# Kernel tuning notes

Measured on AMD Instinct MI355X. Metric: run time of the kernel, lower is better.

The kernel has to match this reference:

```python
import jax, jax.numpy as jnp
import numpy as np

GROUPS = 8
N_HEADS = 8
EPS = 1e-5


def setup_inputs() -> dict:
    key = jax.random.key(0)
    ks = jax.random.split(key, 3)
    B, C, H, W = 8, 512, 32, 32
    x = jax.random.normal(ks[0], (B, C, H, W), dtype=jnp.float32)
    # Conv2d(C, 3C, 1) weight squeezed to [3C, C]; kaiming-ish scale
    qkv_w = jax.random.normal(ks[1], (3 * C, C), dtype=jnp.float32) * (1.0 / np.sqrt(C))
    proj_w = jax.random.normal(ks[2], (C, C), dtype=jnp.float32) * (1.0 / np.sqrt(C))
    return {
        "x": x,
        "norm_gamma": jnp.ones((C,), jnp.float32),
        "norm_beta": jnp.zeros((C,), jnp.float32),
        "qkv_w": qkv_w,
        "qkv_b": jnp.zeros((3 * C,), jnp.float32),
        "proj_w": proj_w,
        "proj_b": jnp.zeros((C,), jnp.float32),
    }


def reference(x, norm_gamma, norm_beta, qkv_w, qkv_b, proj_w, proj_b):
    B, C, H, W = x.shape
    nh = N_HEADS
    hd = C // nh
    scale = hd ** (-0.5)
    S = H * W

    # GroupNorm(8, C): normalize over (C/G, H, W) within each group
    xg = x.reshape(B, GROUPS, -1)
    mean = xg.mean(axis=-1, keepdims=True)
    var = xg.var(axis=-1, keepdims=True)
    xn = ((xg - mean) * jax.lax.rsqrt(var + EPS)).reshape(B, C, H, W)
    xn = xn * norm_gamma[None, :, None, None] + norm_beta[None, :, None, None]

    # 1x1 conv QKV == per-pixel matmul
    qkv = jnp.einsum('oc,bchw->bohw', qkv_w, xn) + qkv_b[None, :, None, None]
    qkv = qkv.reshape(B, 3, nh, hd, S)
    q, k, v = qkv[:, 0], qkv[:, 1], qkv[:, 2]  # each (B, nh, hd, S)

    # attn[b,h,s,t] = sum_d q[b,h,d,s] k[b,h,d,t] * scale
    attn = jax.nn.softmax(jnp.einsum('bhds,bhdt->bhst', q, k) * scale, axis=-1)
    out = jnp.einsum('bhst,bhdt->bhds', attn, v).reshape(B, C, H, W)

    # 1x1 conv projection + residual
    return x + jnp.einsum('oc,bchw->bohw', proj_w, out) + proj_b[None, :, None, None]
```

## Files before the change

kernel.cpp:

```cpp
#include <hip/hip_runtime.h>
#include <hip/hip_bf16.h>

typedef __attribute__((ext_vector_type(4))) float  f32x4;
typedef __attribute__((ext_vector_type(8))) _Float16 f16x8;
typedef __attribute__((ext_vector_type(4))) _Float16 f16x4;
typedef __attribute__((ext_vector_type(2))) __fp16 fp16x2;
typedef __attribute__((ext_vector_type(4))) float  float4v;
typedef __attribute__((ext_vector_type(4))) unsigned int uint4v;

#define BATCH   8
#define CDIM    512
#define SLEN    1024
#define NHEADS  8
#define HDIM    64
#define QSCALE  0.1803368801111f
#define FIXED_M 8.0f


__device__ __forceinline__ float fast_exp2(float x){
    float r;
    asm("v_exp_f32 %0, %1" : "=v"(r) : "v"(x));
    return r;
}

__device__ __forceinline__ void stage16(const void* g, void* l, int lane){
#if __has_builtin(__builtin_amdgcn_global_load_lds)
    __builtin_amdgcn_global_load_lds((const __attribute__((address_space(1))) void*)g,
                                     (__attribute__((address_space(3))) void*)l, 16, 0, 0);
#else
    *(f16x8*)((char*)l + lane * 16) = *(const f16x8*)g;
#endif
}

__device__ __forceinline__ int sigma32(int p){
    return 8 * ((p >> 2) & 3) + 4 * ((p >> 4) & 1) + (p & 3);
}

union PB8 { fp16x2 q[4]; f16x8 v; };


__global__ __launch_bounds__(256) void prep(
    const float4v* __restrict__ qkvw, f16x4* __restrict__ wq,
    const float4v* __restrict__ projw, f16x4* __restrict__ pw,
    const float* __restrict__ x, float* __restrict__ part)
{
    __shared__ float s1[256], s2[256];
    if (blockIdx.x < 1024){
        int i = blockIdx.x * 256 + threadIdx.x;
        if (i < 196608){
            float4v v = qkvw[i];
            wq[i] = (f16x4){ (_Float16)v[0], (_Float16)v[1], (_Float16)v[2], (_Float16)v[3] };
        } else {
            int j = i - 196608;
            float4v v = projw[j];
            pw[j] = (f16x4){ (_Float16)v[0], (_Float16)v[1], (_Float16)v[2], (_Float16)v[3] };
        }
        return;
    }
    int bid = blockIdx.x - 1024;
    int bg = bid >> 3, pc = bid & 7;
    const float4v* xp = (const float4v*)(x + (size_t)bg * 65536 + (size_t)pc * 8192);
    float sum = 0.f, sq = 0.f;
    for (int i = threadIdx.x; i < 2048; i += 256){
        float4v v = xp[i];
        sum += (v[0] + v[1]) + (v[2] + v[3]);
        sq  += (v[0]*v[0] + v[1]*v[1]) + (v[2]*v[2] + v[3]*v[3]);
    }
    s1[threadIdx.x] = sum; s2[threadIdx.x] = sq;
    __syncthreads();
    for (int o = 128; o > 0; o >>= 1){
        if (threadIdx.x < o){ s1[threadIdx.x] += s1[threadIdx.x + o];
                              s2[threadIdx.x] += s2[threadIdx.x + o]; }
        __syncthreads();
    }
    if (threadIdx.x == 0){
        part[bid * 2 + 0] = s1[0];
        part[bid * 2 + 1] = s2[0];
    }
}


__global__ __launch_bounds__(256) void gn_apply(
    const float* __restrict__ x, const float* __restrict__ part,
    const float* __restrict__ gamma, const float* __restrict__ beta,
    _Float16* __restrict__ xnT)
{
    int b = blockIdx.z, g = blockIdx.y, s0 = blockIdx.x * 64;
    int bg = b * 8 + g, c0 = g * 64;

    float sum = 0.f, sq = 0.f;
#pragma unroll
    for (int p = 0; p < 8; p++){
        sum += part[bg * 16 + p * 2 + 0];
        sq  += part[bg * 16 + p * 2 + 1];
    }
    float mean = sum * (1.f / 65536.f);
    float var  = sq  * (1.f / 65536.f) - mean * mean;
    float inv  = rsqrtf(var + 1e-5f);

    __shared__ _Float16 tile[64 * 66];

    int tx = threadIdx.x & 15, ty = threadIdx.x >> 4;
#pragma unroll
    for (int j = 0; j < 4; j++){
        int c = ty + 16 * j;
        float ga = gamma[c0 + c] * inv;
        float be = beta[c0 + c] - mean * ga;
        float4v v = *(const float4v*)(x + ((size_t)(b * CDIM + c0 + c)) * SLEN + s0 + tx * 4);
#pragma unroll
        for (int i = 0; i < 4; i++)
            tile[(tx * 4 + i) * 66 + c] = (_Float16)(v[i] * ga + be);
    }
    __syncthreads();

    int s = threadIdx.x >> 2, cq = (threadIdx.x & 3) * 16;
    const unsigned int* lsrc = (const unsigned int*)((const unsigned short*)tile + s * 66 + cq);
    uint4v lo = { lsrc[0], lsrc[1], lsrc[2], lsrc[3] };
    uint4v hi = { lsrc[4], lsrc[5], lsrc[6], lsrc[7] };
    unsigned int* dst = (unsigned int*)(xnT + ((size_t)b * SLEN + s0 + s) * CDIM + c0 + cq);
    *(uint4v*)dst       = lo;
    *(uint4v*)(dst + 4) = hi;
}


#define GEMM_CORE(APTR, BPTR)                                                   \
    __shared__ __align__(16) char smem[34816];                                  \
    int tid = threadIdx.x;                                                      \
    int wid = tid >> 6, lane = tid & 63;                                        \
    int w0 = wid >> 1, w1 = wid & 1;                                            \
    int lr = lane & 15, lg = lane >> 4;                                         \
    int slotg = ((lane & 3) ^ ((lane >> 3) & 3)) * 16;                          \
    int srow = lane >> 2;                                                       \
    const char* agp = (const char*)(APTR) +                                     \
        ((size_t)(bo + wid * 32 + srow) * CDIM) * 2 + slotg;                    \
    const char* bgp = (const char*)(BPTR) +                                     \
        ((size_t)(sgbase + wid * 32 + srow) * CDIM) * 2 + slotg;                \
    char* lA = smem + wid * 2048;                                               \
    char* lB = smem + 8192 + wid * 2048;                                        \
    f32x4 acc[4][4];                                                            \
    _Pragma("unroll") for (int i = 0; i < 4; i++)                               \
    _Pragma("unroll") for (int j = 0; j < 4; j++)                               \
        acc[i][j] = (f32x4){0.f, 0.f, 0.f, 0.f};                                \
    _Pragma("unroll") for (int j = 0; j < 2; j++){                              \
        stage16(agp + j * 16384, lA + j * 1024, lane);                          \
        stage16(bgp + j * 16384, lB + j * 1024, lane);                          \
    }                                                                           \
    __syncthreads();                                                            \
    int xt = ((lr >> 1) & 3) << 4;                                              \
    for (int it = 0; it < 16; ++it){                                            \
        int cur = (it & 1) * 16384;                                             \
        if (it + 1 < 16){                                                       \
            int nxt = 16384 - cur, ko = (it + 1) * 64;                          \
            _Pragma("unroll") for (int j = 0; j < 2; j++){                      \
                stage16(agp + j * 16384 + ko, lA + nxt + j * 1024, lane);       \
                stage16(bgp + j * 16384 + ko, lB + nxt + j * 1024, lane);       \
            }                                                                   \
        }                                                                       \
        const char* Ac = smem + cur + (w0 * 64 + lr) * 64;                      \
        const char* Bc = smem + cur + 8192 + (w1 * 64 + lr) * 64;               \
        f16x8 af[4], bfr[4];                                                    \
        _Pragma("unroll") for (int t = 0; t < 4; t++){                          \
            af[t]  = *(const f16x8*)(Ac + t * 1024 + ((lg * 16) ^ xt));         \
            bfr[t] = *(const f16x8*)(Bc + t * 1024 + ((lg * 16) ^ xt));         \
        }                                                                       \
        _Pragma("unroll") for (int i = 0; i < 4; i++)                           \
        _Pragma("unroll") for (int j = 0; j < 4; j++)                           \
            acc[i][j] = __builtin_amdgcn_mfma_f32_16x16x32_f16(af[i], bfr[j],   \
                                                               acc[i][j], 0, 0, 0); \
        __syncthreads();                                                        \
    }


__global__ __launch_bounds__(256) void qkv_gemm(
    const _Float16* __restrict__ wq, const _Float16* __restrict__ xnT,
    const float* __restrict__ qkvb,
    _Float16* __restrict__ qT, _Float16* __restrict__ kT, _Float16* __restrict__ vv)
{
    int b  = blockIdx.z;
    int bo = blockIdx.y * 128;
    size_t sgbase = (size_t)b * SLEN + blockIdx.x * 128;

    GEMM_CORE(wq, xnT)

    int obase = bo + w0 * 64, sbase = blockIdx.x * 128 + w1 * 64;
    int p = obase >> 9;
    int h = (obase >> 6) & 7;
    size_t bh = (size_t)b * NHEADS + h;

    if (p == 2){
        _Float16* vt = (_Float16*)(smem + wid * 8704);
#pragma unroll
        for (int i = 0; i < 4; i++){
            int d0 = i * 16 + lg * 4;
            float4v bias = *(const float4v*)(qkvb + obase + d0);
#pragma unroll
            for (int j = 0; j < 4; j++){
                int s_loc = j * 16 + lr;
#pragma unroll
                for (int r = 0; r < 4; r++)
                    vt[(d0 + r) * 68 + s_loc] = (_Float16)(acc[i][j][r] + bias[r]);
            }
        }
        asm volatile("" ::: "memory");
        _Float16* dstv = vv + (bh * HDIM) * SLEN + sbase;
        int dl = lane >> 3, sc8 = (lane & 7) * 8;
#pragma unroll
        for (int m = 0; m < 8; m++){
            int d = m * 8 + dl;
            f16x8 row = *(const f16x8*)(vt + d * 68 + sc8);
            *(f16x8*)(dstv + (size_t)d * SLEN + sc8) = row;
        }
    } else {
        float sc = (p == 0) ? QSCALE : 1.f;
        char* wreg = smem + wid * 8192;
#pragma unroll
        for (int i = 0; i < 4; i++){
            int d0 = i * 16 + lg * 4;
            float4v bias = *(const float4v*)(qkvb + obase + d0);
            int slotbase = (2 * i + (lg >> 1)) * 16;
            int inoff = (lg & 1) * 8;
#pragma unroll
            for (int j = 0; j < 4; j++){
                int s_loc = j * 16 + lr;
                f16x4 pk = { (_Float16)((acc[i][j][0] + bias[0]) * sc),
                             (_Float16)((acc[i][j][1] + bias[1]) * sc),
                             (_Float16)((acc[i][j][2] + bias[2]) * sc),
                             (_Float16)((acc[i][j][3] + bias[3]) * sc) };
                *(f16x4*)(wreg + s_loc * 128 + (slotbase ^ ((s_loc & 7) << 4)) + inoff) = pk;
            }
        }
        asm volatile("" ::: "memory");
        _Float16* dst = (p == 0 ? qT : kT) + (bh * SLEN + sbase) * HDIM;
#pragma unroll
        for (int m = 0; m < 8; m++){
            int s_loc = m * 8 + (lane >> 3);
            f16x8 row = *(const f16x8*)(wreg + s_loc * 128 + (((lane & 7) ^ (s_loc & 7)) << 4));
            *(f16x8*)(dst + (size_t)s_loc * HDIM + (lane & 7) * 8) = row;
        }
    }
}


__global__ __launch_bounds__(256) void proj_gemm(
    const _Float16* __restrict__ pw, const _Float16* __restrict__ outT,
    const float* __restrict__ pb, const float* __restrict__ x,
    float* __restrict__ y)
{
    int b  = blockIdx.z;
    int bo = blockIdx.y * 128;
    size_t sgbase = (size_t)b * SLEN + blockIdx.x * 128;

    GEMM_CORE(pw, outT)

    int obase = bo + w0 * 64, sbase = blockIdx.x * 128 + w1 * 64;
    float* wreg = (float*)(smem + wid * 8704);

#pragma unroll
    for (int half = 0; half < 2; half++){
        asm volatile("" ::: "memory");
#pragma unroll
        for (int jj = 0; jj < 2; jj++){
            int j = half * 2 + jj;
            int srow2 = jj * 16 + lr;
#pragma unroll
            for (int i = 0; i < 4; i++){
                int c0 = i * 16 + lg * 4;
                float4v bias = *(const float4v*)(pb + obase + c0);
                float4v v = { acc[i][j][0] + bias[0], acc[i][j][1] + bias[1],
                              acc[i][j][2] + bias[2], acc[i][j][3] + bias[3] };
                *(float4v*)(wreg + srow2 * 68 + c0) = v;
            }
        }
        asm volatile("" ::: "memory");
        int cl = lane >> 3, sq = (lane & 7) * 4;
#pragma unroll
        for (int g = 0; g < 8; g++){
            int c = cl + 8 * g;
            float r0 = wreg[(sq + 0) * 68 + c];
            float r1 = wreg[(sq + 1) * 68 + c];
            float r2 = wreg[(sq + 2) * 68 + c];
            float r3 = wreg[(sq + 3) * 68 + c];
            size_t idx = ((size_t)b * CDIM + obase + c) * SLEN + sbase + half * 32 + sq;
            float4v xr = *(const float4v*)(x + idx);
            float4v o = { r0 + xr[0], r1 + xr[1], r2 + xr[2], r3 + xr[3] };
            *(float4v*)(y + idx) = o;
        }
    }
}


#define ATTN_CHUNK(c)                                                           \
    {                                                                           \
        const char* kbuf = smem + ((c) & 3) * 16384;                            \
        const char* vbuf = kbuf + 8192;                                         \
        f16x8 kf[4][2];                                                         \
        _Pragma("unroll") for (int i = 0; i < 4; i++){                          \
            const char* kr = kbuf + (16 * i + lr) * 128;                        \
            kf[i][0] = *(const f16x8*)(kr + ((lg * 16) ^ r7));                  \
            kf[i][1] = *(const f16x8*)(kr + ((64 + lg * 16) ^ r7));             \
        }                                                                       \
        f16x8 vf8[2][4];                                                        \
        _Pragma("unroll") for (int ip = 0; ip < 2; ip++)                        \
        _Pragma("unroll") for (int dt = 0; dt < 4; dt++)                        \
            vf8[ip][dt] = *(const f16x8*)(vbuf + (dt * 16 + lr) * 128           \
                                          + ((ip * 64 + lg * 16) ^ r7));        \
        _Pragma("unroll") for (int sj = 0; sj < 2; sj++){                       \
            f32x4 st[4];                                                        \
            _Pragma("unroll") for (int i = 0; i < 4; i++){                      \
                f32x4 z = (f32x4){-FIXED_M, -FIXED_M, -FIXED_M, -FIXED_M};      \
                z = __builtin_amdgcn_mfma_f32_16x16x32_f16(kf[i][0], qf[sj][0], z, 0, 0, 0); \
                z = __builtin_amdgcn_mfma_f32_16x16x32_f16(kf[i][1], qf[sj][1], z, 0, 0, 0); \
                st[i] = z;                                                      \
            }                                                                   \
            PB8 ua, ub;                                                         \
            ua.q[0] = __builtin_amdgcn_cvt_pkrtz(fast_exp2(st[0][0]), fast_exp2(st[0][1])); \
            ua.q[1] = __builtin_amdgcn_cvt_pkrtz(fast_exp2(st[0][2]), fast_exp2(st[0][3])); \
            ua.q[2] = __builtin_amdgcn_cvt_pkrtz(fast_exp2(st[1][0]), fast_exp2(st[1][1])); \
            ua.q[3] = __builtin_amdgcn_cvt_pkrtz(fast_exp2(st[1][2]), fast_exp2(st[1][3])); \
            ub.q[0] = __builtin_amdgcn_cvt_pkrtz(fast_exp2(st[2][0]), fast_exp2(st[2][1])); \
            ub.q[1] = __builtin_amdgcn_cvt_pkrtz(fast_exp2(st[2][2]), fast_exp2(st[2][3])); \
            ub.q[2] = __builtin_amdgcn_cvt_pkrtz(fast_exp2(st[3][0]), fast_exp2(st[3][1])); \
            ub.q[3] = __builtin_amdgcn_cvt_pkrtz(fast_exp2(st[3][2]), fast_exp2(st[3][3])); \
            f16x8 pb8_0 = ua.v, pb8_1 = ub.v;                                   \
            osum[sj] = __builtin_amdgcn_mfma_f32_16x16x32_f16(ones8, pb8_0, osum[sj], 0, 0, 0); \
            osum[sj] = __builtin_amdgcn_mfma_f32_16x16x32_f16(ones8, pb8_1, osum[sj], 0, 0, 0); \
            _Pragma("unroll") for (int dt = 0; dt < 4; dt++){                   \
                f32x4 o = oac[dt][sj];                                          \
                o = __builtin_amdgcn_mfma_f32_16x16x32_f16(vf8[0][dt], pb8_0, o, 0, 0, 0); \
                o = __builtin_amdgcn_mfma_f32_16x16x32_f16(vf8[1][dt], pb8_1, o, 0, 0, 0); \
                oac[dt][sj] = o;                                                \
            }                                                                   \
        }                                                                       \
    }

__global__ __launch_bounds__(256) void attn_kernel(
    const _Float16* __restrict__ qT, const _Float16* __restrict__ kT,
    const _Float16* __restrict__ vv, _Float16* __restrict__ outT)
{
    __shared__ __align__(16) char smem[65536];

    int id = blockIdx.x;
    int h = id & 7, rr = id >> 3;
    int sx = rr & 7, b = rr >> 3;
    size_t bh = (size_t)b * NHEADS + h;
    int tid = threadIdx.x;
    int wid = tid >> 6, lane = tid & 63;
    int lr = lane & 15, lg = lane >> 4;
    int sbase = sx * 128 + wid * 32;
    int phase = sx << 1;

    const _Float16* qp = qT + bh * SLEN * HDIM;
    const _Float16* kp = kT + bh * SLEN * HDIM;
    const _Float16* vp = vv + bh * HDIM * SLEN;

    int r8 = lane >> 3;
    int p0 = wid * 16 + r8;
    int tr0 = 32 * (p0 >> 5) + sigma32(p0 & 31);
    int tr1 = 32 * ((p0 + 8) >> 5) + sigma32((p0 + 8) & 31);
    int scol = ((lane & 7) * 16) ^ ((p0 & 7) << 4);
    const char* kg0 = (const char*)kp + (size_t)tr0 * 128 + scol;
    const char* kg1 = (const char*)kp + (size_t)tr1 * 128 + scol;
    const char* vg  = (const char*)vp + (size_t)p0 * 2048 + scol;
    char* kd = smem + wid * 2048;
    char* vd = smem + 8192 + wid * 2048;

    f16x8 qf[2][2];
#pragma unroll
    for (int sj = 0; sj < 2; sj++)
#pragma unroll
        for (int kk = 0; kk < 2; kk++)
            qf[sj][kk] = *(const f16x8*)(qp + (size_t)(sbase + sj * 16 + lr) * HDIM + kk * 32 + lg * 8);

    f32x4 oac[4][2], osum[2];
#pragma unroll
    for (int dt = 0; dt < 4; dt++){
        oac[dt][0] = (f32x4){0.f, 0.f, 0.f, 0.f};
        oac[dt][1] = (f32x4){0.f, 0.f, 0.f, 0.f};
    }
    osum[0] = (f32x4){0.f, 0.f, 0.f, 0.f};
    osum[1] = (f32x4){0.f, 0.f, 0.f, 0.f};
    const f16x8 ones8 = { (_Float16)1.f, (_Float16)1.f, (_Float16)1.f, (_Float16)1.f,
                          (_Float16)1.f, (_Float16)1.f, (_Float16)1.f, (_Float16)1.f };

#pragma unroll
    for (int c = 0; c < 2; c++){
        int pc = (c + phase) & 15;
        stage16(kg0 + (size_t)pc * 8192, kd + c * 16384,        lane);
        stage16(kg1 + (size_t)pc * 8192, kd + c * 16384 + 1024, lane);
        stage16(vg  + (size_t)pc * 128,          vd + c * 16384,        lane);
        stage16(vg  + (size_t)pc * 128 + 16384,  vd + c * 16384 + 1024, lane);
    }
    __syncthreads();

    int r7 = (lr & 7) << 4;

    for (int cc0 = 0; cc0 < 16; cc0 += 2){
        if (cc0 + 2 < 16){
#pragma unroll
            for (int u = 2; u < 4; u++){
                int lc = cc0 + u, pc = (lc + phase) & 15, bb = (lc & 3) * 16384;
                stage16(kg0 + (size_t)pc * 8192, kd + bb,        lane);
                stage16(kg1 + (size_t)pc * 8192, kd + bb + 1024, lane);
                stage16(vg  + (size_t)pc * 128,          vd + bb,        lane);
                stage16(vg  + (size_t)pc * 128 + 16384,  vd + bb + 1024, lane);
            }
        }
        ATTN_CHUNK(cc0)
        ATTN_CHUNK(cc0 + 1)
        __syncthreads();
    }

#pragma unroll
    for (int sj = 0; sj < 2; sj++){
        float inv = 1.f / osum[sj][0];
        int s = sbase + sj * 16 + lr;
#pragma unroll
        for (int dt = 0; dt < 4; dt++){
            f16x4 ob = { (_Float16)(oac[dt][sj][0] * inv), (_Float16)(oac[dt][sj][1] * inv),
                         (_Float16)(oac[dt][sj][2] * inv), (_Float16)(oac[dt][sj][3] * inv) };
            *(f16x4*)(outT + ((size_t)b * SLEN + s) * CDIM + h * HDIM + dt * 16 + lg * 4) = ob;
        }
    }
}


extern "C" void kernel_launch(void* const* d_in, const int* in_sizes, int n_in,
                              void* d_out, int out_size, void* d_ws, size_t ws_size,
                              hipStream_t stream)
{
    const float* x     = (const float*)d_in[0];
    const float* gamma = (const float*)d_in[1];
    const float* beta  = (const float*)d_in[2];
    const float* qkvw  = (const float*)d_in[3];
    const float* qkvb  = (const float*)d_in[4];
    const float* projw = (const float*)d_in[5];
    const float* projb = (const float*)d_in[6];
    float* out = (float*)d_out;

    char* ws = (char*)d_ws;
    _Float16* wq_bf = (_Float16*)(ws);
    _Float16* pw_bf = (_Float16*)(ws + 1572864);
    _Float16* xnT   = (_Float16*)(ws + 2097152);
    _Float16* qT    = (_Float16*)(ws + 2097152 + 8388608);
    _Float16* kT    = (_Float16*)(ws + 2097152 + 16777216);
    _Float16* vv    = (_Float16*)(ws + 2097152 + 25165824);
    _Float16* outT  = (_Float16*)(ws + 2097152 + 33554432);
    float*    part  = (float*)(ws + 2097152 + 33554432);

    prep<<<1536, 256, 0, stream>>>((const float4v*)qkvw, (f16x4*)wq_bf,
                                   (const float4v*)projw, (f16x4*)pw_bf, x, part);
    gn_apply<<<dim3(16, 8, 8), 256, 0, stream>>>(x, part, gamma, beta, xnT);
    qkv_gemm<<<dim3(8, 12, 8), 256, 0, stream>>>(wq_bf, xnT, qkvb, qT, kT, vv);
    attn_kernel<<<512, 256, 0, stream>>>(qT, kT, vv, outT);
    proj_gemm<<<dim3(8, 4, 8), 256, 0, stream>>>(pw_bf, outT, projb, x, out);
}
```

Baseline: 76.31 us.

## Load attention K/V fragments directly from global memory, dropping LDS staging

The attention kernel no longer stages K and V tiles into shared memory with async global-to-LDS copies and barriers. Each lane now reads its MFMA fragments straight from global memory, relying on L2/L1 reuse across the four waves. To keep that possible, the QKV GEMM epilogue writes K rows in a permuted order, taking over the sigma32 row reordering the staging code used to do. This removes the LDS traffic and __syncthreads, but it gives up the explicit prefetch pipeline, so global-load latency is exposed and each wave now fetches the same data separately.

```diff
diff --git a/kernel.cpp b/kernel.cpp
--- a/kernel.cpp
+++ b/kernel.cpp
@@ -30,10 +30,6 @@
 #else
     *(f16x8*)((char*)l + lane * 16) = *(const f16x8*)g;
 #endif
-}
-
-__device__ __forceinline__ int sigma32(int p){
-    return 8 * ((p >> 2) & 3) + 4 * ((p >> 4) & 1) + (p & 3);
 }
 
 union PB8 { fp16x2 q[4]; f16x8 v; };
@@ -235,7 +231,13 @@
         for (int m = 0; m < 8; m++){
             int s_loc = m * 8 + (lane >> 3);
             f16x8 row = *(const f16x8*)(wreg + s_loc * 128 + (((lane & 7) ^ (s_loc & 7)) << 4));
-            *(f16x8*)(dst + (size_t)s_loc * HDIM + (lane & 7) * 8) = row;
+            int sp = s_loc;
+            if (p == 1){
+                int u = s_loc & 31;
+                sp = (s_loc & 32) | (u & 3) | (((u >> 3) & 1) << 2)
+                     | (((u >> 4) & 1) << 3) | (((u >> 2) & 1) << 4);
+            }
+            *(f16x8*)(dst + (size_t)sp * HDIM + (lane & 7) * 8) = row;
         }
     }
 }
@@ -291,19 +293,17 @@
 
 #define ATTN_CHUNK(c)                                                           \
     {                                                                           \
-        const char* kbuf = smem + ((c) & 3) * 16384;                            \
-        const char* vbuf = kbuf + 8192;                                         \
+        int pc = ((c) + phase) & 15;                                            \
         f16x8 kf[4][2];                                                         \
         _Pragma("unroll") for (int i = 0; i < 4; i++){                          \
-            const char* kr = kbuf + (16 * i + lr) * 128;                        \
-            kf[i][0] = *(const f16x8*)(kr + ((lg * 16) ^ r7));                  \
-            kf[i][1] = *(const f16x8*)(kr + ((64 + lg * 16) ^ r7));             \
+            kf[i][0] = *(const f16x8*)(klane + (size_t)pc * 8192 + i * 2048);   \
+            kf[i][1] = *(const f16x8*)(klane + (size_t)pc * 8192 + i * 2048 + 64); \
         }                                                                       \
         f16x8 vf8[2][4];                                                        \
         _Pragma("unroll") for (int ip = 0; ip < 2; ip++)                        \
         _Pragma("unroll") for (int dt = 0; dt < 4; dt++)                        \
-            vf8[ip][dt] = *(const f16x8*)(vbuf + (dt * 16 + lr) * 128           \
-                                          + ((ip * 64 + lg * 16) ^ r7));        \
+            vf8[ip][dt] = *(const f16x8*)(vlane + (size_t)dt * 32768            \
+                                          + pc * 128 + ip * 64);                \
         _Pragma("unroll") for (int sj = 0; sj < 2; sj++){                       \
             f32x4 st[4];                                                        \
             _Pragma("unroll") for (int i = 0; i < 4; i++){                      \
@@ -337,8 +337,6 @@
     const _Float16* __restrict__ qT, const _Float16* __restrict__ kT,
     const _Float16* __restrict__ vv, _Float16* __restrict__ outT)
 {
-    __shared__ __align__(16) char smem[65536];
-
     int id = blockIdx.x;
     int h = id & 7, rr = id >> 3;
     int sx = rr & 7, b = rr >> 3;
@@ -350,19 +348,8 @@
     int phase = sx << 1;
 
     const _Float16* qp = qT + bh * SLEN * HDIM;
-    const _Float16* kp = kT + bh * SLEN * HDIM;
-    const _Float16* vp = vv + bh * HDIM * SLEN;
-
-    int r8 = lane >> 3;
-    int p0 = wid * 16 + r8;
-    int tr0 = 32 * (p0 >> 5) + sigma32(p0 & 31);
-    int tr1 = 32 * ((p0 + 8) >> 5) + sigma32((p0 + 8) & 31);
-    int scol = ((lane & 7) * 16) ^ ((p0 & 7) << 4);
-    const char* kg0 = (const char*)kp + (size_t)tr0 * 128 + scol;
-    const char* kg1 = (const char*)kp + (size_t)tr1 * 128 + scol;
-    const char* vg  = (const char*)vp + (size_t)p0 * 2048 + scol;
-    char* kd = smem + wid * 2048;
-    char* vd = smem + 8192 + wid * 2048;
+    const char* klane = (const char*)(kT + bh * SLEN * HDIM) + lr * 128 + lg * 16;
+    const char* vlane = (const char*)(vv + bh * HDIM * SLEN) + lr * 2048 + lg * 16;
 
     f16x8 qf[2][2];
 #pragma unroll
@@ -382,32 +369,9 @@
     const f16x8 ones8 = { (_Float16)1.f, (_Float16)1.f, (_Float16)1.f, (_Float16)1.f,
                           (_Float16)1.f, (_Float16)1.f, (_Float16)1.f, (_Float16)1.f };
 
-#pragma unroll
-    for (int c = 0; c < 2; c++){
-        int pc = (c + phase) & 15;
-        stage16(kg0 + (size_t)pc * 8192, kd + c * 16384,        lane);
-        stage16(kg1 + (size_t)pc * 8192, kd + c * 16384 + 1024, lane);
-        stage16(vg  + (size_t)pc * 128,          vd + c * 16384,        lane);
-        stage16(vg  + (size_t)pc * 128 + 16384,  vd + c * 16384 + 1024, lane);
-    }
-    __syncthreads();
-
-    int r7 = (lr & 7) << 4;
-
-    for (int cc0 = 0; cc0 < 16; cc0 += 2){
-        if (cc0 + 2 < 16){
-#pragma unroll
-            for (int u = 2; u < 4; u++){
-                int lc = cc0 + u, pc = (lc + phase) & 15, bb = (lc & 3) * 16384;
-                stage16(kg0 + (size_t)pc * 8192, kd + bb,        lane);
-                stage16(kg1 + (size_t)pc * 8192, kd + bb + 1024, lane);
-                stage16(vg  + (size_t)pc * 128,          vd + bb,        lane);
-                stage16(vg  + (size_t)pc * 128 + 16384,  vd + bb + 1024, lane);
-            }
-        }
-        ATTN_CHUNK(cc0)
-        ATTN_CHUNK(cc0 + 1)
-        __syncthreads();
+#pragma unroll 2
+    for (int cc = 0; cc < 16; cc++){
+        ATTN_CHUNK(cc)
     }
 
 #pragma unroll
```

Result: slower. 111.8 us (+46.5%).
